# Optimization experiments

Measured on AMD Instinct MI355X. Metric: run time of the kernel, lower is better.

## Reference

```python
import jax, jax.numpy as jnp
import numpy as np

ALPHA = 2.0
BIG = 1e10  # stands in for +inf in the min-plus EDT recurrence (avoids inf*0 NaNs)


def _edt_sq_1d_last(f):
    # Exact 1D squared-distance transform along last axis:
    #   out[i] = min_j f[j] + (i - j)^2   (Felzenszwalb-Huttenlocher lower envelope,
    #   computed here as a vectorized min-plus contraction).
    n = f.shape[-1]
    i = jnp.arange(n)
    par = ((i[:, None] - i[None, :]) ** 2).astype(f.dtype)  # [n_out, n_in]
    return jnp.min(f[..., None, :] + par, axis=-1)  # [..., n_out]


def _edt(mask):
    # Exact Euclidean distance transform over axes (1,2,3) of a [B,C,H,W] bool mask:
    # distance from each True pixel to the nearest False pixel (0 on False pixels),
    # matching scipy.ndimage.distance_transform_edt applied per-batch to img[b].
    f = jnp.where(mask, jnp.float32(BIG), jnp.float32(0.0))
    for ax in (1, 2, 3):
        f = jnp.moveaxis(_edt_sq_1d_last(jnp.moveaxis(f, ax, -1)), -1, ax)
    return jnp.sqrt(jnp.minimum(f, BIG))


def _distance_field(img):
    fg = img > 0.5
    fg_any = fg.any(axis=(1, 2, 3))  # original skips samples with empty foreground
    field = _edt(fg) + _edt(~fg)
    return jnp.where(fg_any[:, None, None, None], field, 0.0)


def setup_inputs() -> dict:
    key = jax.random.key(0)
    k1, k2 = jax.random.split(key)
    pred = jax.random.uniform(k1, (4, 1, 256, 256), dtype=jnp.float32)
    # target is a binary segmentation mask in practice
    target = (jax.random.uniform(k2, (4, 1, 256, 256)) > 0.5).astype(jnp.float32)
    return {"pred": pred, "target": target}


def reference(pred, target):
    pred_dt = jax.lax.stop_gradient(_distance_field(pred))      # computed under no_grad
    target_dt = jax.lax.stop_gradient(_distance_field(target))  # computed under no_grad
    pred_error = (pred - target) ** 2
    distance = pred_dt ** ALPHA + target_dt ** ALPHA
    return (pred_error * distance).mean()
```

## Files before the change

kernel.cpp:

```cpp
#include <hip/hip_runtime.h>

#define BIGF 1e10f
#define HH 256
#define WW 256
#define BB 4
#define NPIX (BB * HH * WW)
#define GRID 256
#define MAGIC 0x5F3A9C71u
#define SMAX 16
#define CONV_T 289.0f

#define WS_ACCB_OFF 0
#define WS_RDY_OFF 2048
#define WS_DONE_OFF 3072
#define WS_MASK_OFF 4096

#define LOAD_RLX(p)     __hip_atomic_load((p), __ATOMIC_RELAXED, __HIP_MEMORY_SCOPE_AGENT)
#define STORE_RLX(p, v) __hip_atomic_store((p), (v), __ATOMIC_RELAXED, __HIP_MEMORY_SCOPE_AGENT)

__device__ inline float row_d2(const unsigned* __restrict__ rm, int x, unsigned iv) {
    int wx = x >> 5, bx = x & 31;
    int dl = 1 << 20, dr = 1 << 20;
    unsigned m0 = rm[wx] ^ iv;
    unsigned t = m0 & (0xFFFFFFFFu >> (31 - bx));
    int w = wx;
    while (true) {
        if (t) { int p = (w << 5) + 31 - __builtin_clz(t); dl = x - p; break; }
        if (--w < 0) break;
        t = rm[w] ^ iv;
    }
    t = m0 & (0xFFFFFFFFu << bx);
    w = wx;
    while (true) {
        if (t) { int p = (w << 5) + __builtin_ctz(t); dr = p - x; break; }
        if (++w > 7) break;
        t = rm[w] ^ iv;
    }
    int d = dl < dr ? dl : dr;
    return (d > 255) ? BIGF : (float)(d * d);
}

__device__ inline float col_min(const unsigned* __restrict__ mb, int y, int x, unsigned iv) {
    float best = row_d2(mb + y * 8, x, iv);
    #pragma unroll 1
    for (int s = 1; s < HH; ++s) {
        float ss = (float)(s * s);
        if (ss >= best) break;
        int ym = y - s, yp = y + s;
        if (ym >= 0) best = fminf(best, row_d2(mb + ym * 8, x, iv) + ss);
        if (yp < HH) best = fminf(best, row_d2(mb + yp * 8, x, iv) + ss);
    }
    return best;
}

__device__ inline float col_min_win(const unsigned* __restrict__ mb, int y, int x, unsigned iv) {
    float best = row_d2(mb + y * 8, x, iv);
    #pragma unroll 1
    for (int s = 1; s <= SMAX; ++s) {
        float ss = (float)(s * s);
        if (ss >= best) break;
        int ym = y - s, yp = y + s;
        if (ym >= 0) best = fminf(best, row_d2(mb + ym * 8, x, iv) + ss);
        if (yp < HH) best = fminf(best, row_d2(mb + yp * 8, x, iv) + ss);
    }
    return best;
}

__launch_bounds__(1024, 4)
__global__ void hdt_kernel(const float* __restrict__ pred,
                           const float* __restrict__ tgt,
                           unsigned* __restrict__ gmask,
                           unsigned* __restrict__ ready,
                           unsigned* __restrict__ done,
                           unsigned long long* __restrict__ accb,
                           float* __restrict__ out) {
    int blk = blockIdx.x;
    int b = blk >> 6;
    int tid = threadIdx.x;
    int w = tid >> 6, lane = tid & 63;

    __shared__ __align__(16) unsigned lmask[2][HH][8];
    __shared__ unsigned wfl[16];
    __shared__ float wsum[16];
    __shared__ double dsum[4];

    int x = tid & (WW - 1);
    int y0 = (blk & 63) << 2;
    int yq = y0 + (tid >> 8);
    int idx = (b * HH + yq) * WW + x;
    float pv = pred[idx], tv = tgt[idx];

    {
        int r = ((blk & 63) << 3) + (w >> 1);
        int img = r >> 8, y = r & 255, half = w & 1;
        const float* src = (img ? tgt : pred) + (b * HH + y) * WW + half * 128 + lane;
        unsigned long long b0 = __ballot(src[0] > 0.5f);
        unsigned long long b1 = __ballot(src[64] > 0.5f);
        if (lane == 0) {
            unsigned long long* dst = (unsigned long long*)
                (gmask + ((img * BB + b) * HH + y) * 8 + half * 4);
            STORE_RLX(dst, b0);
            STORE_RLX(dst + 1, b1);
        }
    }

    int ylo = y0 - SMAX; if (ylo < 0) ylo = 0;
    int yhi = y0 + 3 + SMAX; if (yhi > HH - 1) yhi = HH - 1;
    int nrows = yhi - ylo + 1;
    int tot = nrows * 2;
    #pragma unroll 2
    for (int i = w; i < tot; i += 16) {
        int img = (i >= nrows) ? 1 : 0;
        int y = ylo + (img ? i - nrows : i);
        const float* rowp = (img ? tgt : pred) + (b * HH + y) * WW;
        const float4 f = ((const float4*)rowp)[lane];
        unsigned nib = (f.x > 0.5f ? 1u : 0u) | (f.y > 0.5f ? 2u : 0u)
                     | (f.z > 0.5f ? 4u : 0u) | (f.w > 0.5f ? 8u : 0u);
        unsigned v = nib << ((lane & 7) << 2);
        v |= __shfl_xor(v, 1, 64);
        v |= __shfl_xor(v, 2, 64);
        v |= __shfl_xor(v, 4, 64);
        if ((lane & 7) == 0) lmask[img][y][lane >> 3] = v;
    }
    __syncthreads();
    if (tid == 0) STORE_RLX(&ready[blk], MAGIC);

    unsigned ivp = (pv > 0.5f) ? 0xFFFFFFFFu : 0u;
    unsigned ivt = (tv > 0.5f) ? 0xFFFFFFFFu : 0u;
    float bp = col_min_win(&lmask[0][0][0], yq, x, ivp);
    float bt = col_min_win(&lmask[1][0][0], yq, x, ivt);
    bool conv_p = (bp <= CONV_T), conv_t = (bt <= CONV_T);
    float d2p = 0.0f, d2t = 0.0f;
    if (conv_p) { float dt = sqrtf(fminf(bp, BIGF)); d2p = dt * dt; }
    if (conv_t) { float dt = sqrtf(fminf(bt, BIGF)); d2t = dt * dt; }

    unsigned long long fb = __ballot(!(conv_p && conv_t));
    if ((tid & 63) == 0) wfl[w] = (fb != 0ULL) ? 1u : 0u;
    __syncthreads();
    unsigned fb_any = wfl[0] | wfl[1] | wfl[2] | wfl[3] | wfl[4] | wfl[5] | wfl[6]
                    | wfl[7] | wfl[8] | wfl[9] | wfl[10] | wfl[11] | wfl[12]
                    | wfl[13] | wfl[14] | wfl[15];

    if (fb_any) {
        __syncthreads();
        if (tid < 64) {
            while (LOAD_RLX(&ready[(b << 6) + tid]) != MAGIC)
                __builtin_amdgcn_s_sleep(2);
        }
        __syncthreads();
        {
            int img = tid >> 9;
            int row = (tid >> 1) & 255;
            int half = tid & 1;
            const unsigned long long* gp = (const unsigned long long*)
                (gmask + ((img * BB + b) * HH + row) * 8 + half * 4);
            unsigned long long v0 = LOAD_RLX(gp);
            unsigned long long v1 = LOAD_RLX(gp + 1);
            uint4 a = make_uint4((unsigned)v0, (unsigned)(v0 >> 32),
                                 (unsigned)v1, (unsigned)(v1 >> 32));
            ((uint4*)lmask)[tid] = a;
            unsigned onz = a.x | a.y | a.z | a.w;
            unsigned long long bal = __ballot(onz != 0u);
            if ((tid & 63) == 0) wfl[tid >> 6] = (bal != 0ULL) ? 1u : 0u;
        }
        __syncthreads();
        unsigned fl_p = wfl[0] | wfl[1] | wfl[2] | wfl[3] | wfl[4] | wfl[5] | wfl[6] | wfl[7];
        unsigned fl_t = wfl[8] | wfl[9] | wfl[10] | wfl[11] | wfl[12] | wfl[13] | wfl[14] | wfl[15];
        if (!conv_p) {
            d2p = 0.0f;
            if (fl_p) {
                float best = col_min(&lmask[0][0][0], yq, x, ivp);
                float dt = sqrtf(fminf(best, BIGF));
                d2p = dt * dt;
            }
        }
        if (!conv_t) {
            d2t = 0.0f;
            if (fl_t) {
                float best = col_min(&lmask[1][0][0], yq, x, ivt);
                float dt = sqrtf(fminf(best, BIGF));
                d2t = dt * dt;
            }
        }
    }

    float e = pv - tv;
    float lsum = (e * e) * (d2p + d2t);

    #pragma unroll
    for (int off = 32; off > 0; off >>= 1)
        lsum += __shfl_down(lsum, off, 64);
    if ((tid & 63) == 0) wsum[tid >> 6] = lsum;
    __syncthreads();

    if (tid == 0) {
        float s2 = 0.0f;
        #pragma unroll
        for (int i = 0; i < 16; ++i) s2 += wsum[i];
        STORE_RLX(&accb[blk], (unsigned long long)__double_as_longlong((double)s2));
        asm volatile("s_waitcnt vmcnt(0)" ::: "memory");
        STORE_RLX(&done[blk], MAGIC);
    }
    if (blk == 0) {
        double v = 0.0;
        if (tid < GRID) {
            while (LOAD_RLX(&done[tid]) != MAGIC)
                __builtin_amdgcn_s_sleep(2);
            v = __longlong_as_double((long long)LOAD_RLX(&accb[tid]));
        }
        #pragma unroll
        for (int off = 32; off > 0; off >>= 1)
            v += __shfl_down(v, off, 64);
        if (tid < GRID && (tid & 63) == 0) dsum[tid >> 6] = v;
        __syncthreads();
        if (tid == 0)
            out[0] = (float)((dsum[0] + dsum[1] + dsum[2] + dsum[3])
                             * (1.0 / (double)NPIX));
    }
}

extern "C" void kernel_launch(void* const* d_in, const int* in_sizes, int n_in,
                              void* d_out, int out_size, void* d_ws, size_t ws_size,
                              hipStream_t stream) {
    const float* pred = (const float*)d_in[0];
    const float* tgt = (const float*)d_in[1];
    float* out = (float*)d_out;
    char* ws = (char*)d_ws;
    unsigned long long* accb = (unsigned long long*)(ws + WS_ACCB_OFF);
    unsigned* ready = (unsigned*)(ws + WS_RDY_OFF);
    unsigned* done = (unsigned*)(ws + WS_DONE_OFF);
    unsigned* gmask = (unsigned*)(ws + WS_MASK_OFF);

    hdt_kernel<<<GRID, 1024, 0, stream>>>(pred, tgt, gmask, ready, done, accb, out);
}
```

Baseline: 62.81 us.

## Drop global mask exchange, rebuild full masks locally, shrink window, fuse column scans

Removes the cross-block global bitmask publish and the ready-flag spin wait. In the fallback path each block now re-reads and packs the full 256-row pred and target images itself. The local window shrinks from 16 to 8 rows with a matching convergence threshold, and the two column searches are fused into one loop. The change also remaps block IDs to spread batches across XCDs and shortens the final spin sleep. The cost is redundant global reads per block whenever any pixel misses the narrower window, which may now happen more often.

```diff
diff --git a/kernel.cpp b/kernel.cpp
--- a/kernel.cpp
+++ b/kernel.cpp
@@ -7,13 +7,11 @@
 #define NPIX (BB * HH * WW)
 #define GRID 256
 #define MAGIC 0x5F3A9C71u
-#define SMAX 16
-#define CONV_T 289.0f
+#define SMAX 8
+#define CONV_T 81.0f
 
 #define WS_ACCB_OFF 0
-#define WS_RDY_OFF 2048
 #define WS_DONE_OFF 3072
-#define WS_MASK_OFF 4096
 
 #define LOAD_RLX(p)     __hip_atomic_load((p), __ATOMIC_RELAXED, __HIP_MEMORY_SCOPE_AGENT)
 #define STORE_RLX(p, v) __hip_atomic_store((p), (v), __ATOMIC_RELAXED, __HIP_MEMORY_SCOPE_AGENT)
@@ -53,28 +51,47 @@
     return best;
 }
 
-__device__ inline float col_min_win(const unsigned* __restrict__ mb, int y, int x, unsigned iv) {
-    float best = row_d2(mb + y * 8, x, iv);
+__device__ inline void col_min2_win(const unsigned* __restrict__ mb0,
+                                    const unsigned* __restrict__ mb1,
+                                    int y, int x, unsigned iv0, unsigned iv1,
+                                    float& b0, float& b1) {
+    b0 = row_d2(mb0 + y * 8, x, iv0);
+    b1 = row_d2(mb1 + y * 8, x, iv1);
     #pragma unroll 1
     for (int s = 1; s <= SMAX; ++s) {
         float ss = (float)(s * s);
-        if (ss >= best) break;
+        bool d0 = (ss >= b0), d1 = (ss >= b1);
+        if (d0 && d1) break;
         int ym = y - s, yp = y + s;
-        if (ym >= 0) best = fminf(best, row_d2(mb + ym * 8, x, iv) + ss);
-        if (yp < HH) best = fminf(best, row_d2(mb + yp * 8, x, iv) + ss);
-    }
-    return best;
-}
+        if (!d0) {
+            if (ym >= 0) b0 = fminf(b0, row_d2(mb0 + ym * 8, x, iv0) + ss);
+            if (yp < HH) b0 = fminf(b0, row_d2(mb0 + yp * 8, x, iv0) + ss);
+        }
+        if (!d1) {
+            if (ym >= 0) b1 = fminf(b1, row_d2(mb1 + ym * 8, x, iv1) + ss);
+            if (yp < HH) b1 = fminf(b1, row_d2(mb1 + yp * 8, x, iv1) + ss);
+        }
+    }
+}
+
+#define PACK_ROW(rowp, vout)                                                  \
+    {                                                                         \
+        const float4 f = ((const float4*)(rowp))[lane];                       \
+        unsigned nib = (f.x > 0.5f ? 1u : 0u) | (f.y > 0.5f ? 2u : 0u)        \
+                     | (f.z > 0.5f ? 4u : 0u) | (f.w > 0.5f ? 8u : 0u);       \
+        vout = nib << ((lane & 7) << 2);                                      \
+        vout |= __shfl_xor(vout, 1, 64);                                      \
+        vout |= __shfl_xor(vout, 2, 64);                                      \
+        vout |= __shfl_xor(vout, 4, 64);                                      \
+    }
 
 __launch_bounds__(1024, 4)
 __global__ void hdt_kernel(const float* __restrict__ pred,
                            const float* __restrict__ tgt,
-                           unsigned* __restrict__ gmask,
-                           unsigned* __restrict__ ready,
                            unsigned* __restrict__ done,
                            unsigned long long* __restrict__ accb,
                            float* __restrict__ out) {
-    int blk = blockIdx.x;
+    int blk = ((blockIdx.x & 7) << 5) | (blockIdx.x >> 3);
     int b = blk >> 6;
     int tid = threadIdx.x;
     int w = tid >> 6, lane = tid & 63;
@@ -89,20 +106,6 @@
     int yq = y0 + (tid >> 8);
     int idx = (b * HH + yq) * WW + x;
     float pv = pred[idx], tv = tgt[idx];
-
-    {
-        int r = ((blk & 63) << 3) + (w >> 1);
-        int img = r >> 8, y = r & 255, half = w & 1;
-        const float* src = (img ? tgt : pred) + (b * HH + y) * WW + half * 128 + lane;
-        unsigned long long b0 = __ballot(src[0] > 0.5f);
-        unsigned long long b1 = __ballot(src[64] > 0.5f);
-        if (lane == 0) {
-            unsigned long long* dst = (unsigned long long*)
-                (gmask + ((img * BB + b) * HH + y) * 8 + half * 4);
-            STORE_RLX(dst, b0);
-            STORE_RLX(dst + 1, b1);
-        }
-    }
 
     int ylo = y0 - SMAX; if (ylo < 0) ylo = 0;
     int yhi = y0 + 3 + SMAX; if (yhi > HH - 1) yhi = HH - 1;
@@ -113,22 +116,16 @@
         int img = (i >= nrows) ? 1 : 0;
         int y = ylo + (img ? i - nrows : i);
         const float* rowp = (img ? tgt : pred) + (b * HH + y) * WW;
-        const float4 f = ((const float4*)rowp)[lane];
-        unsigned nib = (f.x > 0.5f ? 1u : 0u) | (f.y > 0.5f ? 2u : 0u)
-                     | (f.z > 0.5f ? 4u : 0u) | (f.w > 0.5f ? 8u : 0u);
-        unsigned v = nib << ((lane & 7) << 2);
-        v |= __shfl_xor(v, 1, 64);
-        v |= __shfl_xor(v, 2, 64);
-        v |= __shfl_xor(v, 4, 64);
+        unsigned v;
+        PACK_ROW(rowp, v);
         if ((lane & 7) == 0) lmask[img][y][lane >> 3] = v;
     }
     __syncthreads();
-    if (tid == 0) STORE_RLX(&ready[blk], MAGIC);
 
     unsigned ivp = (pv > 0.5f) ? 0xFFFFFFFFu : 0u;
     unsigned ivt = (tv > 0.5f) ? 0xFFFFFFFFu : 0u;
-    float bp = col_min_win(&lmask[0][0][0], yq, x, ivp);
-    float bt = col_min_win(&lmask[1][0][0], yq, x, ivt);
+    float bp, bt;
+    col_min2_win(&lmask[0][0][0], &lmask[1][0][0], yq, x, ivp, ivt, bp, bt);
     bool conv_p = (bp <= CONV_T), conv_t = (bt <= CONV_T);
     float d2p = 0.0f, d2t = 0.0f;
     if (conv_p) { float dt = sqrtf(fminf(bp, BIGF)); d2p = dt * dt; }
@@ -143,29 +140,24 @@
 
     if (fb_any) {
         __syncthreads();
-        if (tid < 64) {
-            while (LOAD_RLX(&ready[(b << 6) + tid]) != MAGIC)
-                __builtin_amdgcn_s_sleep(2);
-        }
+        unsigned any0 = 0u, any1 = 0u;
+        #pragma unroll 4
+        for (int i = w; i < 512; i += 16) {
+            int img = i >> 8, y = i & 255;
+            const float* rowp = (img ? tgt : pred) + (b * HH + y) * WW;
+            unsigned v;
+            PACK_ROW(rowp, v);
+            if (img) any1 |= v; else any0 |= v;
+            if ((lane & 7) == 0) lmask[img][y][lane >> 3] = v;
+        }
+        unsigned long long A0 = __ballot(any0 != 0u);
+        unsigned long long A1 = __ballot(any1 != 0u);
+        if (lane == 0) wfl[w] = (A0 ? 1u : 0u) | (A1 ? 2u : 0u);
         __syncthreads();
-        {
-            int img = tid >> 9;
-            int row = (tid >> 1) & 255;
-            int half = tid & 1;
-            const unsigned long long* gp = (const unsigned long long*)
-                (gmask + ((img * BB + b) * HH + row) * 8 + half * 4);
-            unsigned long long v0 = LOAD_RLX(gp);
-            unsigned long long v1 = LOAD_RLX(gp + 1);
-            uint4 a = make_uint4((unsigned)v0, (unsigned)(v0 >> 32),
-                                 (unsigned)v1, (unsigned)(v1 >> 32));
-            ((uint4*)lmask)[tid] = a;
-            unsigned onz = a.x | a.y | a.z | a.w;
-            unsigned long long bal = __ballot(onz != 0u);
-            if ((tid & 63) == 0) wfl[tid >> 6] = (bal != 0ULL) ? 1u : 0u;
-        }
-        __syncthreads();
-        unsigned fl_p = wfl[0] | wfl[1] | wfl[2] | wfl[3] | wfl[4] | wfl[5] | wfl[6] | wfl[7];
-        unsigned fl_t = wfl[8] | wfl[9] | wfl[10] | wfl[11] | wfl[12] | wfl[13] | wfl[14] | wfl[15];
+        unsigned m = wfl[0] | wfl[1] | wfl[2] | wfl[3] | wfl[4] | wfl[5] | wfl[6]
+                   | wfl[7] | wfl[8] | wfl[9] | wfl[10] | wfl[11] | wfl[12]
+                   | wfl[13] | wfl[14] | wfl[15];
+        unsigned fl_p = m & 1u, fl_t = m & 2u;
         if (!conv_p) {
             d2p = 0.0f;
             if (fl_p) {
@@ -205,7 +197,7 @@
         double v = 0.0;
         if (tid < GRID) {
             while (LOAD_RLX(&done[tid]) != MAGIC)
-                __builtin_amdgcn_s_sleep(2);
+                __builtin_amdgcn_s_sleep(1);
             v = __longlong_as_double((long long)LOAD_RLX(&accb[tid]));
         }
         #pragma unroll
@@ -227,9 +219,7 @@
     float* out = (float*)d_out;
     char* ws = (char*)d_ws;
     unsigned long long* accb = (unsigned long long*)(ws + WS_ACCB_OFF);
-    unsigned* ready = (unsigned*)(ws + WS_RDY_OFF);
     unsigned* done = (unsigned*)(ws + WS_DONE_OFF);
-    unsigned* gmask = (unsigned*)(ws + WS_MASK_OFF);
-
-    hdt_kernel<<<GRID, 1024, 0, stream>>>(pred, tgt, gmask, ready, done, accb, out);
-}
+
+    hdt_kernel<<<GRID, 1024, 0, stream>>>(pred, tgt, done, accb, out);
+}
```

Measured after the change: 61.10 us. -2.7%, faster.
